# Performance work log

Hardware: AMD Instinct MI355X
Metric: run time of the kernel (lower is better)

## Reference

```python
import jax, jax.numpy as jnp
import numpy as np

TAU = 0.1
N, D = 8192, 128
NUM_CLASSES = 100


def setup_inputs() -> dict:
    key = jax.random.key(0)
    kx, ky = jax.random.split(key)
    x = jax.random.normal(kx, (N, D), dtype=jnp.float32)
    y = jax.random.randint(ky, (N,), 0, NUM_CLASSES, dtype=jnp.int64)
    return {"x": x, "y": y}


def reference(x, y):
    # cosine similarity matrix: S[i,j] = <x_i, x_j> / (||x_i|| ||x_j||)
    norms = jnp.linalg.norm(x, axis=-1, keepdims=True)  # [N,1]
    xn = x / norms
    sim = jnp.einsum('id,jd->ij', xn, xn)               # [N,N]
    e = jnp.exp(sim / TAU)                              # [N,N]
    same = (y[:, None] == y[None, :])                   # [N,N] bool (includes self, as in original)
    top = jnp.sum(jnp.where(same, e, 0.0), axis=1)      # [N]
    down = jnp.sum(e, axis=1)                           # [N]
    loss = jnp.mean(-jnp.log(top / down))
    return loss
```

## Files before the change

kernel.cpp:

```cpp
#include <hip/hip_runtime.h>
#include <hip/hip_bf16.h>
#include <stdint.h>

#define NROWS 8192
#define DDIM  128
#define NCHUNK 16
#define ROWS_PER_BLOCK 128
#define COLS_PER_BLOCK 512
#define GROUP_COLS 64
#define GROUP_BYTES (GROUP_COLS * DDIM * 2)
#define NGROUPS (COLS_PER_BLOCK / GROUP_COLS)

typedef __attribute__((ext_vector_type(8))) short short8;
typedef __attribute__((ext_vector_type(4))) float f32x4;

__device__ __forceinline__ void load_lds16(const void* g, void* l) {
    __builtin_amdgcn_global_load_lds(
        (const __attribute__((address_space(1))) void*)g,
        (__attribute__((address_space(3))) void*)l, 16, 0, 0);
}

#define SCALE 14.426950408889634f

__global__ __launch_bounds__(256) void normalize_kernel(
    const float* __restrict__ x, __hip_bfloat16* __restrict__ q)
{
    int wave = threadIdx.x >> 6;
    int lane = threadIdx.x & 63;
    int row  = blockIdx.x * 4 + wave;
    const float* xr = x + (size_t)row * DDIM;
    float a = xr[lane];
    float b = xr[lane + 64];
    float ss = a * a + b * b;
    #pragma unroll
    for (int off = 1; off < 64; off <<= 1)
        ss += __shfl_xor(ss, off, 64);
    float rn = sqrtf(SCALE) / sqrtf(ss);
    q[(size_t)row * DDIM + lane]      = __float2bfloat16(a * rn);
    q[(size_t)row * DDIM + lane + 64] = __float2bfloat16(b * rn);
}

__global__ __launch_bounds__(256, 4) void sim_kernel(
    const __hip_bfloat16* __restrict__ q, const int* __restrict__ y,
    float* __restrict__ topp, float* __restrict__ downp)
{
    __shared__ char smem[2 * GROUP_BYTES];
    __shared__ int  yl[COLS_PER_BLOCK];

    const int bid  = blockIdx.x;
    const int iblk = bid >> 4;
    const int h    = bid & 15;
    const int tid  = threadIdx.x;
    const int wave = tid >> 6;
    const int lane = tid & 63;
    const int lrow = lane & 15;
    const int lhi  = lane >> 4;

    const char* qb = (const char*)q;
    const int rbase = iblk * ROWS_PER_BLOCK + wave * 32;
    const int jbase = h * COLS_PER_BLOCK;

    yl[tid]       = y[jbase + tid];
    yl[tid + 256] = y[jbase + tid + 256];

    short8 afrag[2][4];
    #pragma unroll
    for (int t = 0; t < 2; ++t)
        #pragma unroll
        for (int ks = 0; ks < 4; ++ks)
            afrag[t][ks] = *(const short8*)(qb +
                (size_t)(rbase + t * 16 + lrow) * 256 + ks * 64 + lhi * 16);

    int yrow[2][4];
    #pragma unroll
    for (int t = 0; t < 2; ++t)
        #pragma unroll
        for (int r = 0; r < 4; ++r)
            yrow[t][r] = y[rbase + t * 16 + lhi * 4 + r];

    float top[2][4]  = {{0.f,0.f,0.f,0.f},{0.f,0.f,0.f,0.f}};
    float down[2][4] = {{0.f,0.f,0.f,0.f},{0.f,0.f,0.f,0.f}};

    auto stage = [&](int buf, int g) {
        const int jstart = jbase + g * GROUP_COLS;
        #pragma unroll
        for (int p = 0; p < 4; ++p) {
            int phys = p * 4096 + wave * 1024 + lane * 16;
            int L = phys ^ (((phys >> 8) & 7) << 4);
            const char* src = qb + (size_t)(jstart + (L >> 8)) * 256 + (L & 255);
            load_lds16(src, smem + buf * GROUP_BYTES + p * 4096 + wave * 1024);
        }
    };

    stage(0, 0);
    __syncthreads();

    for (int g = 0; g < NGROUPS; ++g) {
        if (g + 1 < NGROUPS) stage((g + 1) & 1, g + 1);

        const char* lbuf = smem + (g & 1) * GROUP_BYTES;

        #pragma unroll
        for (int jt = 0; jt < 4; ++jt) {
            const int cg = jt * 16 + lrow;
            const int ycol = yl[g * GROUP_COLS + cg];
            short8 bfrag[4];
            #pragma unroll
            for (int ks = 0; ks < 4; ++ks) {
                int L = cg * 256 + ks * 64 + lhi * 16;
                int phys = L ^ ((cg & 7) << 4);
                bfrag[ks] = *(const short8*)(lbuf + phys);
            }
            #pragma unroll
            for (int t = 0; t < 2; ++t) {
                f32x4 acc = {0.f, 0.f, 0.f, 0.f};
                #pragma unroll
                for (int ks = 0; ks < 4; ++ks)
                    acc = __builtin_amdgcn_mfma_f32_16x16x32_bf16(
                        afrag[t][ks], bfrag[ks], acc, 0, 0, 0);
                #pragma unroll
                for (int r = 0; r < 4; ++r) {
                    float e = __builtin_amdgcn_exp2f(acc[r]);
                    down[t][r] += e;
                    if (yrow[t][r] == ycol) top[t][r] += e;
                }
            }
        }
        __syncthreads();
    }

    #pragma unroll
    for (int m = 1; m < 16; m <<= 1) {
        #pragma unroll
        for (int t = 0; t < 2; ++t)
            #pragma unroll
            for (int r = 0; r < 4; ++r) {
                top[t][r]  += __shfl_xor(top[t][r],  m, 64);
                down[t][r] += __shfl_xor(down[t][r], m, 64);
            }
    }

    if (lrow == 0) {
        #pragma unroll
        for (int t = 0; t < 2; ++t)
            #pragma unroll
            for (int r = 0; r < 4; ++r) {
                int row = rbase + t * 16 + lhi * 4 + r;
                topp [h * NROWS + row] = top[t][r];
                downp[h * NROWS + row] = down[t][r];
            }
    }
}

__global__ __launch_bounds__(64) void loss_partial_kernel(
    const float* __restrict__ topp, const float* __restrict__ downp,
    float* __restrict__ partial)
{
    const int lane = threadIdx.x;
    const int r = blockIdx.x * 64 + lane;
    float t = 0.f, d = 0.f;
    #pragma unroll
    for (int hh = 0; hh < NCHUNK; ++hh) {
        t += topp [hh * NROWS + r];
        d += downp[hh * NROWS + r];
    }
    float s = __logf(d) - __logf(t);
    #pragma unroll
    for (int off = 1; off < 64; off <<= 1)
        s += __shfl_xor(s, off, 64);
    if (lane == 0) partial[blockIdx.x] = s;
}

__global__ __launch_bounds__(64) void loss_final_kernel(
    const float* __restrict__ partial, float* __restrict__ out)
{
    const int lane = threadIdx.x;
    float s = partial[lane] + partial[lane + 64];
    #pragma unroll
    for (int off = 1; off < 64; off <<= 1)
        s += __shfl_xor(s, off, 64);
    if (lane == 0) out[0] = s / (float)NROWS;
}

extern "C" void kernel_launch(void* const* d_in, const int* in_sizes, int n_in,
                              void* d_out, int out_size, void* d_ws, size_t ws_size,
                              hipStream_t stream)
{
    const float* x = (const float*)d_in[0];
    const int*   y = (const int*)d_in[1];
    float* out = (float*)d_out;

    char* ws = (char*)d_ws;
    __hip_bfloat16* q = (__hip_bfloat16*)ws;
    float* topp  = (float*)(ws + (size_t)NROWS * DDIM * 2);
    float* downp = topp + NCHUNK * NROWS;
    float* partial = downp + NCHUNK * NROWS;

    normalize_kernel<<<NROWS / 4, 256, 0, stream>>>(x, q);
    sim_kernel<<<64 * NCHUNK, 256, 0, stream>>>(q, y, topp, downp);
    loss_partial_kernel<<<NROWS / 64, 64, 0, stream>>>(topp, downp, partial);
    loss_final_kernel<<<1, 64, 0, stream>>>(partial, out);
}
```

Measured before the change: 41.74 us.

## Load B fragments directly from global memory instead of LDS double-buffering

Removes the LDS staging of column tiles (global_load_lds with swizzle and per-group barriers) and has each wave read its B fragments straight from global/L2, relying on cache reuse across the four waves. This drops the per-group __syncthreads and the LDS traffic, and frees LDS for occupancy. In exchange each wave issues redundant global loads for the same columns and has no explicit prefetch, so latency hiding depends on the compiler and on occupancy. The conditional top accumulate is also rewritten as a select.

```diff
diff --git a/kernel.cpp b/kernel.cpp
--- a/kernel.cpp
+++ b/kernel.cpp
@@ -7,18 +7,9 @@
 #define NCHUNK 16
 #define ROWS_PER_BLOCK 128
 #define COLS_PER_BLOCK 512
-#define GROUP_COLS 64
-#define GROUP_BYTES (GROUP_COLS * DDIM * 2)
-#define NGROUPS (COLS_PER_BLOCK / GROUP_COLS)
 
 typedef __attribute__((ext_vector_type(8))) short short8;
 typedef __attribute__((ext_vector_type(4))) float f32x4;
-
-__device__ __forceinline__ void load_lds16(const void* g, void* l) {
-    __builtin_amdgcn_global_load_lds(
-        (const __attribute__((address_space(1))) void*)g,
-        (__attribute__((address_space(3))) void*)l, 16, 0, 0);
-}
 
 #define SCALE 14.426950408889634f
 
@@ -44,8 +35,7 @@
     const __hip_bfloat16* __restrict__ q, const int* __restrict__ y,
     float* __restrict__ topp, float* __restrict__ downp)
 {
-    __shared__ char smem[2 * GROUP_BYTES];
-    __shared__ int  yl[COLS_PER_BLOCK];
+    __shared__ int yl[COLS_PER_BLOCK];
 
     const int bid  = blockIdx.x;
     const int iblk = bid >> 4;
@@ -78,55 +68,35 @@
         for (int r = 0; r < 4; ++r)
             yrow[t][r] = y[rbase + t * 16 + lhi * 4 + r];
 
+    __syncthreads();
+
     float top[2][4]  = {{0.f,0.f,0.f,0.f},{0.f,0.f,0.f,0.f}};
     float down[2][4] = {{0.f,0.f,0.f,0.f},{0.f,0.f,0.f,0.f}};
 
-    auto stage = [&](int buf, int g) {
-        const int jstart = jbase + g * GROUP_COLS;
+    #pragma unroll 2
+    for (int jt = 0; jt < COLS_PER_BLOCK / 16; ++jt) {
+        const int cg = jt * 16 + lrow;
+        const char* bsrc = qb + (size_t)(jbase + cg) * 256 + lhi * 16;
+        short8 bfrag[4];
         #pragma unroll
-        for (int p = 0; p < 4; ++p) {
-            int phys = p * 4096 + wave * 1024 + lane * 16;
-            int L = phys ^ (((phys >> 8) & 7) << 4);
-            const char* src = qb + (size_t)(jstart + (L >> 8)) * 256 + (L & 255);
-            load_lds16(src, smem + buf * GROUP_BYTES + p * 4096 + wave * 1024);
-        }
-    };
-
-    stage(0, 0);
-    __syncthreads();
-
-    for (int g = 0; g < NGROUPS; ++g) {
-        if (g + 1 < NGROUPS) stage((g + 1) & 1, g + 1);
-
-        const char* lbuf = smem + (g & 1) * GROUP_BYTES;
+        for (int ks = 0; ks < 4; ++ks)
+            bfrag[ks] = *(const short8*)(bsrc + ks * 64);
+        const int ycol = yl[cg];
 
         #pragma unroll
-        for (int jt = 0; jt < 4; ++jt) {
-            const int cg = jt * 16 + lrow;
-            const int ycol = yl[g * GROUP_COLS + cg];
-            short8 bfrag[4];
+        for (int t = 0; t < 2; ++t) {
+            f32x4 acc = {0.f, 0.f, 0.f, 0.f};
             #pragma unroll
-            for (int ks = 0; ks < 4; ++ks) {
-                int L = cg * 256 + ks * 64 + lhi * 16;
-                int phys = L ^ ((cg & 7) << 4);
-                bfrag[ks] = *(const short8*)(lbuf + phys);
-            }
+            for (int ks = 0; ks < 4; ++ks)
+                acc = __builtin_amdgcn_mfma_f32_16x16x32_bf16(
+                    afrag[t][ks], bfrag[ks], acc, 0, 0, 0);
             #pragma unroll
-            for (int t = 0; t < 2; ++t) {
-                f32x4 acc = {0.f, 0.f, 0.f, 0.f};
-                #pragma unroll
-                for (int ks = 0; ks < 4; ++ks)
-                    acc = __builtin_amdgcn_mfma_f32_16x16x32_bf16(
-                        afrag[t][ks], bfrag[ks], acc, 0, 0, 0);
-                #pragma unroll
-                for (int r = 0; r < 4; ++r) {
-                    float e = __builtin_amdgcn_exp2f(acc[r]);
-                    down[t][r] += e;
-                    if (yrow[t][r] == ycol) top[t][r] += e;
-                }
+            for (int r = 0; r < 4; ++r) {
+                float e = __builtin_amdgcn_exp2f(acc[r]);
+                down[t][r] += e;
+                top[t][r]  += (yrow[t][r] == ycol) ? e : 0.0f;
             }
         }
-        __syncthreads();
     }
 
     #pragma unroll
```

After: 76.92 us. 1.84x slower.

## Switch similarity GEMM to FP8 MFMA with exact diagonal self-term correction

Applied to the files above, without the earlier changes.

Normalized rows are quantized to FP8 instead of bf16. This halves the operand bytes moved through global memory and LDS and uses the fp8 MFMA instruction. To limit error on the dominant diagonal term, the normalize kernel stores each row's quantized self-dot. The loss kernel then subtracts exp2 of that value and adds the exact exp(1/tau) in its place. Off-diagonal similarities still carry FP8 rounding error, which risks accuracy against the reference tolerance.

```diff
diff --git a/kernel.cpp b/kernel.cpp
--- a/kernel.cpp
+++ b/kernel.cpp
@@ -8,11 +8,11 @@
 #define ROWS_PER_BLOCK 128
 #define COLS_PER_BLOCK 512
 #define GROUP_COLS 64
-#define GROUP_BYTES (GROUP_COLS * DDIM * 2)
+#define GROUP_BYTES (GROUP_COLS * DDIM)
 #define NGROUPS (COLS_PER_BLOCK / GROUP_COLS)
 
-typedef __attribute__((ext_vector_type(8))) short short8;
 typedef __attribute__((ext_vector_type(4))) float f32x4;
+typedef long f8x8;
 
 __device__ __forceinline__ void load_lds16(const void* g, void* l) {
     __builtin_amdgcn_global_load_lds(
@@ -21,27 +21,35 @@
 }
 
 #define SCALE 14.426950408889634f
+#define E10   22026.465794806718f
 
 __global__ __launch_bounds__(256) void normalize_kernel(
-    const float* __restrict__ x, __hip_bfloat16* __restrict__ q)
+    const float* __restrict__ x, unsigned short* __restrict__ q16,
+    float* __restrict__ dsq)
 {
     int wave = threadIdx.x >> 6;
     int lane = threadIdx.x & 63;
     int row  = blockIdx.x * 4 + wave;
-    const float* xr = x + (size_t)row * DDIM;
-    float a = xr[lane];
-    float b = xr[lane + 64];
-    float ss = a * a + b * b;
+    const float2* xr = (const float2*)(x + (size_t)row * DDIM);
+    float2 v = xr[lane];
+    float ss = v.x * v.x + v.y * v.y;
     #pragma unroll
     for (int off = 1; off < 64; off <<= 1)
         ss += __shfl_xor(ss, off, 64);
-    float rn = sqrtf(SCALE) / sqrtf(ss);
-    q[(size_t)row * DDIM + lane]      = __float2bfloat16(a * rn);
-    q[(size_t)row * DDIM + lane + 64] = __float2bfloat16(b * rn);
+    float rn = sqrtf(SCALE / ss);
+    int pk = __builtin_amdgcn_cvt_pk_fp8_f32(v.x * rn, v.y * rn, 0, false);
+    q16[(size_t)row * 64 + lane] = (unsigned short)(pk & 0xffff);
+    float d0 = __builtin_amdgcn_cvt_f32_fp8(pk, 0);
+    float d1 = __builtin_amdgcn_cvt_f32_fp8(pk, 1);
+    float sq = d0 * d0 + d1 * d1;
+    #pragma unroll
+    for (int off = 1; off < 64; off <<= 1)
+        sq += __shfl_xor(sq, off, 64);
+    if (lane == 0) dsq[row] = sq;
 }
 
 __global__ __launch_bounds__(256, 4) void sim_kernel(
-    const __hip_bfloat16* __restrict__ q, const int* __restrict__ y,
+    const unsigned short* __restrict__ q16, const int* __restrict__ y,
     float* __restrict__ topp, float* __restrict__ downp)
 {
     __shared__ char smem[2 * GROUP_BYTES];
@@ -51,25 +59,25 @@
     const int iblk = bid >> 4;
     const int h    = bid & 15;
     const int tid  = threadIdx.x;
+    const int lane = tid & 63;
     const int wave = tid >> 6;
-    const int lane = tid & 63;
     const int lrow = lane & 15;
     const int lhi  = lane >> 4;
 
-    const char* qb = (const char*)q;
+    const char* qb = (const char*)q16;
     const int rbase = iblk * ROWS_PER_BLOCK + wave * 32;
     const int jbase = h * COLS_PER_BLOCK;
 
     yl[tid]       = y[jbase + tid];
     yl[tid + 256] = y[jbase + tid + 256];
 
-    short8 afrag[2][4];
+    f8x8 afrag[2][4];
     #pragma unroll
     for (int t = 0; t < 2; ++t)
         #pragma unroll
         for (int ks = 0; ks < 4; ++ks)
-            afrag[t][ks] = *(const short8*)(qb +
-                (size_t)(rbase + t * 16 + lrow) * 256 + ks * 64 + lhi * 16);
+            afrag[t][ks] = *(const f8x8*)(qb +
+                (size_t)(rbase + t * 16 + lrow) * DDIM + ks * 32 + lhi * 8);
 
     int yrow[2][4];
     #pragma unroll
@@ -84,11 +92,12 @@
     auto stage = [&](int buf, int g) {
         const int jstart = jbase + g * GROUP_COLS;
         #pragma unroll
-        for (int p = 0; p < 4; ++p) {
-            int phys = p * 4096 + wave * 1024 + lane * 16;
-            int L = phys ^ (((phys >> 8) & 7) << 4);
-            const char* src = qb + (size_t)(jstart + (L >> 8)) * 256 + (L & 255);
-            load_lds16(src, smem + buf * GROUP_BYTES + p * 4096 + wave * 1024);
+        for (int p = 0; p < 2; ++p) {
+            int phys = p * 4096 + tid * 16;
+            int col  = phys >> 7;
+            int L    = phys ^ ((col & 7) << 4);
+            const char* src = qb + (size_t)(jstart + col) * DDIM + (L & 127);
+            load_lds16(src, smem + buf * GROUP_BYTES + phys);
         }
     };
 
@@ -101,28 +110,27 @@
         const char* lbuf = smem + (g & 1) * GROUP_BYTES;
 
         #pragma unroll
-        for (int jt = 0; jt < 4; ++jt) {
+        for (int jt = 0; jt < GROUP_COLS / 16; ++jt) {
             const int cg = jt * 16 + lrow;
             const int ycol = yl[g * GROUP_COLS + cg];
-            short8 bfrag[4];
+            f8x8 bfrag[4];
             #pragma unroll
             for (int ks = 0; ks < 4; ++ks) {
-                int L = cg * 256 + ks * 64 + lhi * 16;
-                int phys = L ^ ((cg & 7) << 4);
-                bfrag[ks] = *(const short8*)(lbuf + phys);
+                int off = cg * DDIM + ((ks * 32 + lhi * 8) ^ ((cg & 7) << 4));
+                bfrag[ks] = *(const f8x8*)(lbuf + off);
             }
             #pragma unroll
             for (int t = 0; t < 2; ++t) {
                 f32x4 acc = {0.f, 0.f, 0.f, 0.f};
                 #pragma unroll
                 for (int ks = 0; ks < 4; ++ks)
-                    acc = __builtin_amdgcn_mfma_f32_16x16x32_bf16(
+                    acc = __builtin_amdgcn_mfma_f32_16x16x32_fp8_fp8(
                         afrag[t][ks], bfrag[ks], acc, 0, 0, 0);
                 #pragma unroll
                 for (int r = 0; r < 4; ++r) {
                     float e = __builtin_amdgcn_exp2f(acc[r]);
                     down[t][r] += e;
-                    if (yrow[t][r] == ycol) top[t][r] += e;
+                    top[t][r]  += (yrow[t][r] == ycol) ? e : 0.0f;
                 }
             }
         }
@@ -154,7 +162,7 @@
 
 __global__ __launch_bounds__(64) void loss_partial_kernel(
     const float* __restrict__ topp, const float* __restrict__ downp,
-    float* __restrict__ partial)
+    const float* __restrict__ dsq, float* __restrict__ partial)
 {
     const int lane = threadIdx.x;
     const int r = blockIdx.x * 64 + lane;
@@ -164,6 +172,9 @@
         t += topp [hh * NROWS + r];
         d += downp[hh * NROWS + r];
     }
+    float e2d = __builtin_amdgcn_exp2f(dsq[r]);
+    t = t - e2d + E10;
+    d = d - e2d + E10;
     float s = __logf(d) - __logf(t);
     #pragma unroll
     for (int off = 1; off < 64; off <<= 1)
@@ -191,13 +202,14 @@
     float* out = (float*)d_out;
 
     char* ws = (char*)d_ws;
-    __hip_bfloat16* q = (__hip_bfloat16*)ws;
-    float* topp  = (float*)(ws + (size_t)NROWS * DDIM * 2);
+    unsigned short* q16 = (unsigned short*)ws;
+    float* topp  = (float*)(ws + (size_t)NROWS * DDIM);
     float* downp = topp + NCHUNK * NROWS;
-    float* partial = downp + NCHUNK * NROWS;
-
-    normalize_kernel<<<NROWS / 4, 256, 0, stream>>>(x, q);
-    sim_kernel<<<64 * NCHUNK, 256, 0, stream>>>(q, y, topp, downp);
-    loss_partial_kernel<<<NROWS / 64, 64, 0, stream>>>(topp, downp, partial);
+    float* dsq     = downp + NCHUNK * NROWS;
+    float* partial = dsq + NROWS;
+
+    normalize_kernel<<<NROWS / 4, 256, 0, stream>>>(x, q16, dsq);
+    sim_kernel<<<64 * NCHUNK, 256, 0, stream>>>(q16, y, topp, downp);
+    loss_partial_kernel<<<NROWS / 64, 64, 0, stream>>>(topp, downp, dsq, partial);
     loss_final_kernel<<<1, 64, 0, stream>>>(partial, out);
 }
```

New measurement: 36.30 us. 1.15x faster.
